# Kernel tuning notes

Measured on AMD Instinct MI355X. Metric: run time of the kernel, lower is better.

Reference implementation:

```python
import jax, jax.numpy as jnp
import numpy as np
import math

B, CIN, COUT, H, W, K, SDIM = 8, 512, 512, 64, 64, 3, 512
EPS = 1e-8
NEG_SLOPE = 0.2
SCALE = math.sqrt(2.0)


def setup_inputs() -> dict:
    key = jax.random.key(0)
    ks = jax.random.split(key, 7)
    x = jax.random.normal(ks[0], (B, CIN, H, W), jnp.float32)
    style = jax.random.normal(ks[1], (B, SDIM), jnp.float32)
    noise = jax.random.normal(ks[2], (B, 1, H, W), jnp.float32)
    # kernel stored as (kh, kw, Cin, Cout) like keras Conv2D
    fan_in = K * K * CIN
    kernel = jax.random.normal(ks[3], (K, K, CIN, COUT), jnp.float32) / math.sqrt(fan_in)
    style_scale = jax.random.normal(ks[4], (SDIM, COUT), jnp.float32) * 0.02
    bias = jax.random.normal(ks[5], (COUT,), jnp.float32) * 0.01
    noise_weight = jax.random.normal(ks[6], (1,), jnp.float32) * 0.1
    return {"x": x, "style": style, "noise": noise, "kernel": kernel,
            "style_scale": style_scale, "bias": bias, "noise_weight": noise_weight}


def _styled_conv(x, style, noise, kernel, style_scale, bias, noise_weight):
    b = x.shape[0]
    # --- modulation ---
    s = style @ style_scale                              # [B, Cout]
    w = kernel[None] * (s[:, None, None, None, :] + 1.0)  # [B, kh, kw, Cin, Cout]
    # --- demodulation ---
    d = jax.lax.rsqrt(jnp.sum(jnp.square(w), axis=(1, 2, 3)) + EPS)  # [B, Cout]
    w = w * d[:, None, None, None, :]
    # --- per-sample conv via batch-as-groups trick ---
    # weights -> OIHW with O = B*Cout, groups = B
    w_oihw = jnp.transpose(w, (0, 4, 3, 1, 2)).reshape(b * COUT, CIN, K, K)
    x_g = x.reshape(1, b * CIN, H, W)
    out = jax.lax.conv_general_dilated(
        x_g, w_oihw, window_strides=(1, 1), padding="SAME",
        feature_group_count=b,
        dimension_numbers=("NCHW", "OIHW", "NCHW"))
    out = out.reshape(b, COUT, H, W)
    # --- noise injection ---
    out = out + noise_weight[0] * noise                  # noise broadcasts over channels
    # --- fused bias + leaky relu * sqrt(2) ---
    out = jax.nn.leaky_relu(out + bias[None, :, None, None], NEG_SLOPE) * SCALE
    return out


def reference(x, style, noise, kernel, style_scale, bias, noise_weight):
    return _styled_conv(x, style, noise, kernel, style_scale, bias, noise_weight)
```

## Files before the change

### kernel.cpp

```cpp
#include <hip/hip_runtime.h>

#define B_     8
#define CIN_   512
#define COUT_  512
#define HW_    64
#define SDIM_  512
#define NPIX   4096
#define KTOT   4608
#define PADW   66

typedef __attribute__((ext_vector_type(4))) float f32x4;
typedef __attribute__((ext_vector_type(8))) short bf16x8;
typedef __attribute__((ext_vector_type(8))) unsigned short u16x8;

__device__ __forceinline__ float bf2f(unsigned short b) {
    unsigned int u = ((unsigned int)b) << 16;
    return __builtin_bit_cast(float, u);
}
__device__ __forceinline__ unsigned short f2bf(float f) {
    unsigned int u = __builtin_bit_cast(unsigned int, f);
    return (unsigned short)((u + 0x7fffu + ((u >> 16) & 1u)) >> 16);
}
__device__ __forceinline__ float ldin(const void* p, size_t i, int isbf) {
    return isbf ? bf2f(((const unsigned short*)p)[i]) : ((const float*)p)[i];
}

#define GLD16(g, l) __builtin_amdgcn_global_load_lds( \
    (__attribute__((address_space(1))) void*)(g),     \
    (__attribute__((address_space(3))) void*)(l), 16, 0, 0)

__global__ void detect_dtype(const unsigned int* __restrict__ style_u32,
                             int* __restrict__ flag) {
    int t = threadIdx.x;
    unsigned int w = style_u32[t * 4];
    int e = (w >> 7) & 0xFF;
    int isbf = (e >= 110 && e <= 140) ? 1 : 0;
    __shared__ int cnt;
    if (t == 0) cnt = 0;
    __syncthreads();
    atomicAdd(&cnt, isbf);
    __syncthreads();
    if (t == 0) *flag = (cnt >= 128) ? 1 : 0;
}

__global__ void halo_zero(unsigned int* __restrict__ xtp2u) {
    int idx = blockIdx.x;
    int b = blockIdx.y;
    int y, x;
    if (idx < 66)       { y = 0;  x = idx; }
    else if (idx < 132) { y = 65; x = idx - 66; }
    else if (idx < 196) { x = 0;  y = idx - 131; }
    else                { x = 65; y = idx - 195; }
    int t = threadIdx.x;
    int cit = t >> 5, j = t & 31;
    size_t u32i = ((((size_t)(b * 8 + cit) * 66 + y) * 66 + x) << 5) + j;
    xtp2u[u32i] = 0;
}

__global__ void wt_transpose(const void* __restrict__ kin,
                             unsigned short* __restrict__ wt,
                             const int* __restrict__ flag) {
    __shared__ __align__(16) unsigned short tile[64][72];
    int isbf = *flag;
    int t = threadIdx.x;
    int co0 = blockIdx.x * 64;
    int k0  = blockIdx.y * 64;
    int r = t >> 2, c16 = (t & 3) << 4;
    if (isbf) {
        const unsigned short* src = (const unsigned short*)kin + (size_t)(k0 + r) * COUT_ + co0 + c16;
        *(u16x8*)&tile[r][c16]     = *(const u16x8*)src;
        *(u16x8*)&tile[r][c16 + 8] = *(const u16x8*)(src + 8);
    } else {
        const float* src = (const float*)kin + (size_t)(k0 + r) * COUT_ + co0 + c16;
#pragma unroll
        for (int q = 0; q < 4; ++q) {
            f32x4 v = *(const f32x4*)(src + q * 4);
#pragma unroll
            for (int j = 0; j < 4; ++j) tile[r][c16 + q * 4 + j] = f2bf(v[j]);
        }
    }
    __syncthreads();
    int c = t >> 2, r16 = (t & 3) << 4;
    u16x8 w0, w1;
#pragma unroll
    for (int j = 0; j < 8; ++j) { w0[j] = tile[r16 + j][c]; w1[j] = tile[r16 + 8 + j][c]; }
    unsigned short* dst = wt + (size_t)(co0 + c) * KTOT + k0 + r16;
    *(u16x8*)dst       = w0;
    *(u16x8*)(dst + 8) = w1;
}

__global__ void xpose(const void* __restrict__ x,
                      unsigned short* __restrict__ xtp2,
                      const int* __restrict__ flag) {
    __shared__ __align__(16) unsigned short tile[64][72];
    int isbf = *flag;
    int t = threadIdx.x;
    int cit = blockIdx.x;
    int y   = blockIdx.y;
    int b   = blockIdx.z;
    int ci_l = t >> 2, xo = (t & 3) << 4;
    size_t srcoff = (((size_t)(b * CIN_ + cit * 64 + ci_l)) * HW_ + y) * HW_ + xo;
    if (isbf) {
        const unsigned short* src = (const unsigned short*)x + srcoff;
        *(u16x8*)&tile[ci_l][xo]     = *(const u16x8*)src;
        *(u16x8*)&tile[ci_l][xo + 8] = *(const u16x8*)(src + 8);
    } else {
        const float* src = (const float*)x + srcoff;
#pragma unroll
        for (int q = 0; q < 4; ++q) {
            f32x4 v = *(const f32x4*)(src + q * 4);
#pragma unroll
            for (int j = 0; j < 4; ++j) tile[ci_l][xo + q * 4 + j] = f2bf(v[j]);
        }
    }
    __syncthreads();
    int xl = t >> 2, cio = (t & 3) << 4;
    u16x8 w0, w1;
#pragma unroll
    for (int j = 0; j < 8; ++j) { w0[j] = tile[cio + j][xl]; w1[j] = tile[cio + 8 + j][xl]; }
    unsigned short* dst =
        xtp2 + ((((size_t)(b * 8 + cit) * 66 + (y + 1)) * 66 + (xl + 1)) << 6) + cio;
    *(u16x8*)dst       = w0;
    *(u16x8*)(dst + 8) = w1;
}

__global__ void mod_kernel(const void* __restrict__ style,
                           const void* __restrict__ sscale,
                           const unsigned short* __restrict__ wt,
                           float* __restrict__ mmod,
                           const int* __restrict__ flag) {
    int isbf = *flag;
    int co = blockIdx.x, t = threadIdx.x;
    int lane = t & 63, wid = t >> 6;
    float k2 = 0.f;
    const unsigned short* wr = wt + (size_t)co * KTOT;
    for (int k = t; k < KTOT; k += 256) { float v = bf2f(wr[k]); k2 += v * v; }
    float sb[B_];
#pragma unroll
    for (int b = 0; b < B_; ++b) sb[b] = 0.f;
    for (int sd = t; sd < SDIM_; sd += 256) {
        float ss = ldin(sscale, (size_t)sd * COUT_ + co, isbf);
#pragma unroll
        for (int b = 0; b < B_; ++b) sb[b] += ldin(style, b * SDIM_ + sd, isbf) * ss;
    }
    __shared__ float red[4][9];
    float vals[9];
    vals[0] = k2;
#pragma unroll
    for (int b = 0; b < B_; ++b) vals[1 + b] = sb[b];
#pragma unroll
    for (int q = 0; q < 9; ++q) {
        float v = vals[q];
        for (int off = 32; off; off >>= 1) v += __shfl_down(v, off);
        if (lane == 0) red[wid][q] = v;
    }
    __syncthreads();
    if (t < B_) {
        int b = t;
        float k2t = red[0][0] + red[1][0] + red[2][0] + red[3][0];
        float s   = red[0][1 + b] + red[1][1 + b] + red[2][1 + b] + red[3][1 + b];
        float sp1 = s + 1.f;
        mmod[b * COUT_ + co] = sp1 * rsqrtf(sp1 * sp1 * k2t + 1e-8f);
    }
}

__global__ __launch_bounds__(512, 2) void conv_gemm(
    const unsigned short* __restrict__ wt,
    const unsigned short* __restrict__ xtp2,
    const float* __restrict__ mmod,
    const void* __restrict__ noise,
    const void* __restrict__ bias,
    const void* __restrict__ nwp,
    void* __restrict__ out,
    const int* __restrict__ flag) {
    __shared__ __align__(1024) unsigned short Asm[2][256 * 64];
    __shared__ __align__(1024) unsigned short Win[6 * 72 * 64];
    int isbf = *flag;
    int tid = threadIdx.x;
    int lane = tid & 63, wid = tid >> 6;
    int lr = lane & 15, hi = lane >> 4;
    int wm = wid >> 2, wn = wid & 3;

    int bid = blockIdx.x;
    int swz = (bid & 7) * 32 + (bid >> 3);
    int gy = swz >> 7;
    int nb = swz & 127;
    int b  = nb >> 4;
    int nt = nb & 15;
    int pl0 = nt << 8;
    int h0  = pl0 >> 6;
    int co0 = gy << 8;

    f32x4 acc[8][4];
#pragma unroll
    for (int i = 0; i < 8; ++i)
#pragma unroll
        for (int j = 0; j < 4; ++j) acc[i][j] = (f32x4){0.f, 0.f, 0.f, 0.f};

    int rsub = lane >> 3;
    int ce_src = ((lane & 7) ^ rsub) << 3;
    int swzr = (lane & 7) << 3;
    int wsrc = (rsub << 6) + (((lane & 7) ^ (rsub & 7)) << 3);
    int l7 = lane & 7;
    int px[4];
#pragma unroll
    for (int ni = 0; ni < 4; ++ni) px[ni] = ((ni << 4) + lr) << 6;

    auto stageA = [&](int koff, int pp, int q) {
        const unsigned short* srcA =
            wt + (size_t)(co0 + (q << 6) + (wid << 3) + rsub) * KTOT + koff + ce_src;
        GLD16(srcA, (char*)&Asm[pp][0] + (q << 13) + (wid << 10));
    };
    auto stage_win = [&](int cit) {
        size_t base = ((size_t)(b * 8 + cit) * 66 + h0) * (66 * 64);
        for (int idx = wid; idx < 54; idx += 8) {
            int r = idx / 9, g = idx - r * 9;
            const unsigned short* src = xtp2 + base + (size_t)r * (66 * 64) + (g << 9) + wsrc;
            GLD16(src, (char*)Win + r * 9216 + (g << 10));
        }
    };

    stage_win(0);
#pragma unroll
    for (int q = 0; q < 4; ++q) stageA(0, 0, q);
    asm volatile("s_waitcnt vmcnt(0)" ::: "memory");
    __builtin_amdgcn_s_barrier();
    asm volatile("" ::: "memory");

    int t = 0;
    for (int cit = 0; cit < 8; ++cit) {
        if (cit > 0) {
            stage_win(cit);
            asm volatile("s_waitcnt vmcnt(0)" ::: "memory");
            __builtin_amdgcn_s_barrier();
            asm volatile("" ::: "memory");
        }
        for (int khw = 0; khw < 9; ++khw, ++t) {
            int p = t & 1, pn = p ^ 1;
            const unsigned short* As = &Asm[p][0];
            int kh = (khw >= 6) ? 2 : ((khw >= 3) ? 1 : 0);
            int kw = khw - kh * 3;
            int BD = (((wn + kh) * 72) + kw) << 6;
            int xv = ((l7 + kw) & 7) << 3;

            if (t < 71) {
                int khw1 = (khw == 8) ? 0 : khw + 1;
                int cit1 = (khw == 8) ? cit + 1 : cit;
                int koff1 = khw1 * 512 + (cit1 << 6);
#pragma unroll
                for (int q = 0; q < 4; ++q) stageA(koff1, pn, q);
            }

            int kc0 = (hi << 3), kc1 = 32 + (hi << 3);
            bf16x8 a0[4], bk0[4], a1[4], a2[4], bk1[4], a3[4];
#pragma unroll
            for (int i = 0; i < 4; ++i)
                a0[i] = *(const bf16x8*)&As[(((wm << 7) + (i << 4) + lr) << 6) + (kc0 ^ swzr)];
#pragma unroll
            for (int ni = 0; ni < 4; ++ni)
                bk0[ni] = *(const bf16x8*)&Win[BD + px[ni] + (kc0 ^ xv)];
#pragma unroll
            for (int i = 0; i < 4; ++i)
                a1[i] = *(const bf16x8*)&As[(((wm << 7) + ((i + 4) << 4) + lr) << 6) + (kc0 ^ swzr)];
#pragma unroll
            for (int i = 0; i < 4; ++i)
                a2[i] = *(const bf16x8*)&As[(((wm << 7) + (i << 4) + lr) << 6) + (kc1 ^ swzr)];
#pragma unroll
            for (int ni = 0; ni < 4; ++ni)
                bk1[ni] = *(const bf16x8*)&Win[BD + px[ni] + (kc1 ^ xv)];
#pragma unroll
            for (int i = 0; i < 4; ++i)
                a3[i] = *(const bf16x8*)&As[(((wm << 7) + ((i + 4) << 4) + lr) << 6) + (kc1 ^ swzr)];

#pragma unroll
            for (int mf = 0; mf < 4; ++mf)
#pragma unroll
                for (int nf = 0; nf < 4; ++nf)
                    acc[mf][nf] = __builtin_amdgcn_mfma_f32_16x16x32_bf16(a0[mf], bk0[nf], acc[mf][nf], 0, 0, 0);
#pragma unroll
            for (int mf = 0; mf < 4; ++mf)
#pragma unroll
                for (int nf = 0; nf < 4; ++nf)
                    acc[mf + 4][nf] = __builtin_amdgcn_mfma_f32_16x16x32_bf16(a1[mf], bk0[nf], acc[mf + 4][nf], 0, 0, 0);
#pragma unroll
            for (int mf = 0; mf < 4; ++mf)
#pragma unroll
                for (int nf = 0; nf < 4; ++nf)
                    acc[mf][nf] = __builtin_amdgcn_mfma_f32_16x16x32_bf16(a2[mf], bk1[nf], acc[mf][nf], 0, 0, 0);
#pragma unroll
            for (int mf = 0; mf < 4; ++mf)
#pragma unroll
                for (int nf = 0; nf < 4; ++nf)
                    acc[mf + 4][nf] = __builtin_amdgcn_mfma_f32_16x16x32_bf16(a3[mf], bk1[nf], acc[mf + 4][nf], 0, 0, 0);

            __builtin_amdgcn_sched_group_barrier(0x010, 4, 0);
            __builtin_amdgcn_sched_group_barrier(0x100, 8, 0);
#pragma unroll
            for (int r = 0; r < 4; ++r) {
                __builtin_amdgcn_sched_group_barrier(0x100, 1, 0);
                __builtin_amdgcn_sched_group_barrier(0x008, 4, 0);
            }
#pragma unroll
            for (int r = 0; r < 8; ++r) {
                __builtin_amdgcn_sched_group_barrier(0x100, 1, 0);
                __builtin_amdgcn_sched_group_barrier(0x008, 2, 0);
            }
#pragma unroll
            for (int r = 0; r < 4; ++r) {
                __builtin_amdgcn_sched_group_barrier(0x100, 1, 0);
                __builtin_amdgcn_sched_group_barrier(0x008, 4, 0);
            }
            __builtin_amdgcn_sched_group_barrier(0x008, 16, 0);

            asm volatile("s_waitcnt lgkmcnt(0)" ::: "memory");
            if (t < 71) asm volatile("s_waitcnt vmcnt(0)" ::: "memory");
            __builtin_amdgcn_s_barrier();
            asm volatile("" ::: "memory");
        }
    }

    float nw = ldin(nwp, 0, isbf);
    unsigned short* out16 = (unsigned short*)out;
    float* outf = (float*)out;
#pragma unroll
    for (int mf = 0; mf < 8; ++mf) {
        int cobase = co0 + (wm << 7) + (mf << 4) + (hi << 2);
        f32x4 mv = *(const f32x4*)&mmod[b * COUT_ + cobase];
        float bb[4];
#pragma unroll
        for (int r = 0; r < 4; ++r) bb[r] = ldin(bias, cobase + r, isbf);
#pragma unroll
        for (int nf = 0; nf < 4; ++nf) {
            int pix = pl0 + (wn << 6) + (nf << 4) + lr;
            float nv = nw * ldin(noise, b * NPIX + pix, isbf);
#pragma unroll
            for (int r = 0; r < 4; ++r) {
                float v = acc[mf][nf][r] * mv[r] + nv + bb[r];
                v = (v < 0.f ? v * 0.2f : v) * 1.41421356237f;
                size_t oidx = ((size_t)(b * COUT_ + cobase + r)) * NPIX + pix;
                if (isbf) out16[oidx] = f2bf(v);
                else      outf[oidx]  = v;
            }
        }
    }
}

extern "C" void kernel_launch(void* const* d_in, const int* in_sizes, int n_in,
                              void* d_out, int out_size, void* d_ws, size_t ws_size,
                              hipStream_t stream) {
    const void* x      = d_in[0];
    const void* style  = d_in[1];
    const void* noise  = d_in[2];
    const void* kin    = d_in[3];
    const void* sscale = d_in[4];
    const void* bias   = d_in[5];
    const void* nwp    = d_in[6];

    char* ws = (char*)d_ws;
    int* flag = (int*)ws;
    const size_t xtp_off   = 256;
    const size_t xtp_bytes = (size_t)B_ * 8 * 66 * 66 * 64 * 2;
    const size_t pad       = 4096;
    const size_t wt_bytes  = (size_t)COUT_ * KTOT * 2;
    unsigned short* xtp2 = (unsigned short*)(ws + xtp_off);
    unsigned short* wtr  = (unsigned short*)(ws + xtp_off + xtp_bytes + pad);
    float* mmod          = (float*)(ws + xtp_off + xtp_bytes + pad + wt_bytes);

    detect_dtype<<<1, 256, 0, stream>>>((const unsigned int*)style, flag);
    halo_zero<<<dim3(260, 8), 256, 0, stream>>>((unsigned int*)xtp2);
    wt_transpose<<<dim3(8, 72), 256, 0, stream>>>(kin, wtr, flag);
    xpose<<<dim3(8, 64, 8), 256, 0, stream>>>(x, xtp2, flag);
    mod_kernel<<<512, 256, 0, stream>>>(style, sscale, wtr, mmod, flag);
    conv_gemm<<<256, 512, 0, stream>>>(wtr, xtp2, mmod, noise, bias, nwp, d_out, flag);
}
```

Measured before the change: 182.1 us.

## Split conv GEMM tile across 16 waves with 1024-thread blocks

Doubles the conv_gemm block to 1024 threads. Each wave now computes a 64x64 output sub-tile instead of 128x64, so the accumulator array and A-fragment registers are halved. The A-tile staging, window staging stride, MFMA schedule hints and epilogue are re-indexed for 16 waves. The aim is more waves per CU to hide latency, at the cost of more LDS reads per MFMA because each B fragment is reused over fewer A rows. The aggressive launch bounds may also cap registers and cause spills.

```diff
diff --git a/kernel.cpp b/kernel.cpp
--- a/kernel.cpp
+++ b/kernel.cpp
@@ -164,7 +164,7 @@
     }
 }
 
-__global__ __launch_bounds__(512, 2) void conv_gemm(
+__global__ __launch_bounds__(1024, 4) void conv_gemm(
     const unsigned short* __restrict__ wt,
     const unsigned short* __restrict__ xtp2,
     const float* __restrict__ mmod,
@@ -191,9 +191,9 @@
     int h0  = pl0 >> 6;
     int co0 = gy << 8;
 
-    f32x4 acc[8][4];
-#pragma unroll
-    for (int i = 0; i < 8; ++i)
+    f32x4 acc[4][4];
+#pragma unroll
+    for (int i = 0; i < 4; ++i)
 #pragma unroll
         for (int j = 0; j < 4; ++j) acc[i][j] = (f32x4){0.f, 0.f, 0.f, 0.f};
 
@@ -206,14 +206,15 @@
 #pragma unroll
     for (int ni = 0; ni < 4; ++ni) px[ni] = ((ni << 4) + lr) << 6;
 
-    auto stageA = [&](int koff, int pp, int q) {
+    auto stageA = [&](int koff, int pp, int j) {
+        int row0 = ((wid << 1) + j) << 3;
         const unsigned short* srcA =
-            wt + (size_t)(co0 + (q << 6) + (wid << 3) + rsub) * KTOT + koff + ce_src;
-        GLD16(srcA, (char*)&Asm[pp][0] + (q << 13) + (wid << 10));
+            wt + (size_t)(co0 + row0 + rsub) * KTOT + koff + ce_src;
+        GLD16(srcA, (char*)&Asm[pp][0] + (row0 << 7));
     };
     auto stage_win = [&](int cit) {
         size_t base = ((size_t)(b * 8 + cit) * 66 + h0) * (66 * 64);
-        for (int idx = wid; idx < 54; idx += 8) {
+        for (int idx = wid; idx < 54; idx += 16) {
             int r = idx / 9, g = idx - r * 9;
             const unsigned short* src = xtp2 + base + (size_t)r * (66 * 64) + (g << 9) + wsrc;
             GLD16(src, (char*)Win + r * 9216 + (g << 10));
@@ -221,8 +222,7 @@
     };
 
     stage_win(0);
-#pragma unroll
-    for (int q = 0; q < 4; ++q) stageA(0, 0, q);
+    stageA(0, 0, 0); stageA(0, 0, 1);
     asm volatile("s_waitcnt vmcnt(0)" ::: "memory");
     __builtin_amdgcn_s_barrier();
     asm volatile("" ::: "memory");
@@ -247,30 +247,23 @@
                 int khw1 = (khw == 8) ? 0 : khw + 1;
                 int cit1 = (khw == 8) ? cit + 1 : cit;
                 int koff1 = khw1 * 512 + (cit1 << 6);
-#pragma unroll
-                for (int q = 0; q < 4; ++q) stageA(koff1, pn, q);
+                stageA(koff1, pn, 0); stageA(koff1, pn, 1);
             }
 
             int kc0 = (hi << 3), kc1 = 32 + (hi << 3);
-            bf16x8 a0[4], bk0[4], a1[4], a2[4], bk1[4], a3[4];
+            bf16x8 a0[4], bk0[4], a1[4], bk1[4];
 #pragma unroll
             for (int i = 0; i < 4; ++i)
-                a0[i] = *(const bf16x8*)&As[(((wm << 7) + (i << 4) + lr) << 6) + (kc0 ^ swzr)];
+                a0[i] = *(const bf16x8*)&As[(((wm << 6) + (i << 4) + lr) << 6) + (kc0 ^ swzr)];
 #pragma unroll
             for (int ni = 0; ni < 4; ++ni)
                 bk0[ni] = *(const bf16x8*)&Win[BD + px[ni] + (kc0 ^ xv)];
 #pragma unroll
             for (int i = 0; i < 4; ++i)
-                a1[i] = *(const bf16x8*)&As[(((wm << 7) + ((i + 4) << 4) + lr) << 6) + (kc0 ^ swzr)];
-#pragma unroll
-            for (int i = 0; i < 4; ++i)
-                a2[i] = *(const bf16x8*)&As[(((wm << 7) + (i << 4) + lr) << 6) + (kc1 ^ swzr)];
+                a1[i] = *(const bf16x8*)&As[(((wm << 6) + (i << 4) + lr) << 6) + (kc1 ^ swzr)];
 #pragma unroll
             for (int ni = 0; ni < 4; ++ni)
                 bk1[ni] = *(const bf16x8*)&Win[BD + px[ni] + (kc1 ^ xv)];
-#pragma unroll
-            for (int i = 0; i < 4; ++i)
-                a3[i] = *(const bf16x8*)&As[(((wm << 7) + ((i + 4) << 4) + lr) << 6) + (kc1 ^ swzr)];
 
 #pragma unroll
             for (int mf = 0; mf < 4; ++mf)
@@ -281,35 +274,15 @@
             for (int mf = 0; mf < 4; ++mf)
 #pragma unroll
                 for (int nf = 0; nf < 4; ++nf)
-                    acc[mf + 4][nf] = __builtin_amdgcn_mfma_f32_16x16x32_bf16(a1[mf], bk0[nf], acc[mf + 4][nf], 0, 0, 0);
-#pragma unroll
-            for (int mf = 0; mf < 4; ++mf)
-#pragma unroll
-                for (int nf = 0; nf < 4; ++nf)
-                    acc[mf][nf] = __builtin_amdgcn_mfma_f32_16x16x32_bf16(a2[mf], bk1[nf], acc[mf][nf], 0, 0, 0);
-#pragma unroll
-            for (int mf = 0; mf < 4; ++mf)
-#pragma unroll
-                for (int nf = 0; nf < 4; ++nf)
-                    acc[mf + 4][nf] = __builtin_amdgcn_mfma_f32_16x16x32_bf16(a3[mf], bk1[nf], acc[mf + 4][nf], 0, 0, 0);
-
-            __builtin_amdgcn_sched_group_barrier(0x010, 4, 0);
+                    acc[mf][nf] = __builtin_amdgcn_mfma_f32_16x16x32_bf16(a1[mf], bk1[nf], acc[mf][nf], 0, 0, 0);
+
+            __builtin_amdgcn_sched_group_barrier(0x010, 2, 0);
             __builtin_amdgcn_sched_group_barrier(0x100, 8, 0);
-#pragma unroll
-            for (int r = 0; r < 4; ++r) {
-                __builtin_amdgcn_sched_group_barrier(0x100, 1, 0);
-                __builtin_amdgcn_sched_group_barrier(0x008, 4, 0);
-            }
 #pragma unroll
             for (int r = 0; r < 8; ++r) {
                 __builtin_amdgcn_sched_group_barrier(0x100, 1, 0);
                 __builtin_amdgcn_sched_group_barrier(0x008, 2, 0);
             }
-#pragma unroll
-            for (int r = 0; r < 4; ++r) {
-                __builtin_amdgcn_sched_group_barrier(0x100, 1, 0);
-                __builtin_amdgcn_sched_group_barrier(0x008, 4, 0);
-            }
             __builtin_amdgcn_sched_group_barrier(0x008, 16, 0);
 
             asm volatile("s_waitcnt lgkmcnt(0)" ::: "memory");
@@ -323,8 +296,8 @@
     unsigned short* out16 = (unsigned short*)out;
     float* outf = (float*)out;
 #pragma unroll
-    for (int mf = 0; mf < 8; ++mf) {
-        int cobase = co0 + (wm << 7) + (mf << 4) + (hi << 2);
+    for (int mf = 0; mf < 4; ++mf) {
+        int cobase = co0 + (wm << 6) + (mf << 4) + (hi << 2);
         f32x4 mv = *(const f32x4*)&mmod[b * COUT_ + cobase];
         float bb[4];
 #pragma unroll
@@ -371,5 +344,5 @@
     wt_transpose<<<dim3(8, 72), 256, 0, stream>>>(kin, wtr, flag);
     xpose<<<dim3(8, 64, 8), 256, 0, stream>>>(x, xtp2, flag);
     mod_kernel<<<512, 256, 0, stream>>>(style, sscale, wtr, mmod, flag);
-    conv_gemm<<<256, 512, 0, stream>>>(wtr, xtp2, mmod, noise, bias, nwp, d_out, flag);
-}
+    conv_gemm<<<256, 1024, 0, stream>>>(wtr, xtp2, mmod, noise, bias, nwp, d_out, flag);
+}
```

Result: slower. 192.6 us (+5.8%).
